# Kernel optimization log

Hardware: AMD Instinct MI355X
Metric: run time of the kernel (lower is better)

The kernel has to match this reference:

```python
import jax, jax.numpy as jnp
import numpy as np

N, E, G, B, L = 24576, 98304, 512, 512, 1000
F_IN, H1, C1, C2, HID = 5, 2, 64, 128, 256


def setup_inputs() -> dict:
    key = jax.random.key(0)
    ks = jax.random.split(key, 20)
    rn = lambda k, s: jax.random.normal(k, s, jnp.float32) * 0.1
    return {
        "x": jax.random.normal(ks[0], (N, F_IN), jnp.float32),
        "edge_index": jax.random.randint(ks[1], (2, E), 0, N),
        "batch": jnp.sort(jax.random.randint(ks[2], (N,), 0, G)),
        "protein_seq": jax.random.randint(ks[3], (B, L), 0, 22),
        "W1": rn(ks[4], (F_IN, H1 * C1)), "att_src1": rn(ks[5], (H1, C1)), "att_dst1": rn(ks[6], (H1, C1)), "b1": jnp.zeros((H1 * C1,), jnp.float32),
        "W2": rn(ks[7], (H1 * C1, C2)), "att_src2": rn(ks[8], (1, C2)), "att_dst2": rn(ks[9], (1, C2)), "b2": jnp.zeros((C2,), jnp.float32),
        "Wd": rn(ks[10], (C2, HID)), "bd": jnp.zeros((HID,), jnp.float32),
        "Pe": rn(ks[11], (22, 64)),
        "K1": rn(ks[12], (64, 64, 3)), "bk1": jnp.zeros((64,), jnp.float32),
        "K2": rn(ks[13], (128, 64, 5)), "bk2": jnp.zeros((128,), jnp.float32),
        "Wp": rn(ks[14], (128, HID)), "bp": jnp.zeros((HID,), jnp.float32),
        "Wf1": rn(ks[15], (2 * HID, 128)), "bf1": jnp.zeros((128,), jnp.float32),
        "Wf2": rn(ks[16], (128, 64)), "bf2": jnp.zeros((64,), jnp.float32),
        "Wo": rn(ks[17], (64, 1)), "bo": jnp.zeros((1,), jnp.float32),
    }


def _gat(x, edge_index, W, att_src, att_dst, b, heads, out_ch):
    """PyG GATConv: add self-loops, per-edge LeakyReLU(0.2) scores, segment softmax over dst."""
    n = x.shape[0]
    h = (x @ W).reshape(n, heads, out_ch)
    loop = jnp.arange(n)
    src = jnp.concatenate([edge_index[0], loop])
    dst = jnp.concatenate([edge_index[1], loop])
    a_s = jnp.sum(h * att_src[None], axis=-1)  # [n, H]
    a_d = jnp.sum(h * att_dst[None], axis=-1)
    e = jax.nn.leaky_relu(a_s[src] + a_d[dst], negative_slope=0.2)  # [E+n, H]
    m = jax.ops.segment_max(e, dst, num_segments=n)
    w = jnp.exp(e - m[dst])
    den = jax.ops.segment_sum(w, dst, num_segments=n)
    alpha = w / (den[dst] + 1e-16)
    out = jax.ops.segment_sum(h[src] * alpha[..., None], dst, num_segments=n)
    return out.reshape(n, heads * out_ch) + b


def _conv1d(x, k, pad):  # x: [B,C,L], k: [O,I,K]
    return jax.lax.conv_general_dilated(x, k, (1,), [(pad, pad)], dimension_numbers=("NCH", "OIH", "NCH"))


def reference(x, edge_index, batch, protein_seq, W1, att_src1, att_dst1, b1, W2, att_src2, att_dst2, b2, Wd, bd, Pe, K1, bk1, K2, bk2, Wp, bp, Wf1, bf1, Wf2, bf2, Wo, bo):
    # drug branch (GAT x2 + global mean pool)
    g = jax.nn.elu(_gat(x, edge_index, W1, att_src1, att_dst1, b1, H1, C1))
    g = jax.nn.elu(_gat(g, edge_index, W2, att_src2, att_dst2, b2, 1, C2))
    sums = jax.ops.segment_sum(g, batch, num_segments=G)
    cnt = jax.ops.segment_sum(jnp.ones((g.shape[0], 1), g.dtype), batch, num_segments=G)
    drug = jax.nn.relu(sums / jnp.maximum(cnt, 1.0) @ Wd + bd)
    # protein branch (embed -> conv1d x2 -> global max pool)
    pe = Pe[protein_seq].transpose(0, 2, 1)  # [B, 64, L]
    p = jax.nn.elu(_conv1d(pe, K1, 1) + bk1[None, :, None])
    p = jax.nn.elu(_conv1d(p, K2, 2) + bk2[None, :, None])
    prot = jax.nn.relu(jnp.max(p, axis=2) @ Wp + bp)
    # head
    h = jnp.concatenate([drug, prot], axis=1)
    h = jax.nn.relu(h @ Wf1 + bf1)
    h = jax.nn.relu(h @ Wf2 + bf2)
    return h @ Wo + bo
```

## Files before the change

### kernel.cpp

```cpp
#include <hip/hip_runtime.h>
#include <hip/hip_bf16.h>
#include <math.h>

#define NN 24576
#define NE 98304
#define ETOT (NE + NN)
#define NG 512
#define NB 512
#define LL 1000
#define TL 60
#define NTILE 17
#define PROT_BLKS (NB * NTILE)
#define CNT_BLKS (ETOT / 256)
#define AS1_BLKS (NN * 2 / 256)

typedef __attribute__((ext_vector_type(8))) short short8;
typedef __attribute__((ext_vector_type(4))) short short4v;
typedef __attribute__((ext_vector_type(4))) float f32x4;

__device__ inline short f2bf(float x) {
    union { __hip_bfloat16 b; short s; } u;
    u.b = __float2bfloat16(x);
    return u.s;
}

__device__ inline float bf2f(short s) {
    return __uint_as_float(((unsigned)(unsigned short)s) << 16);
}

__global__ void k_init_prep(int* deg, int* cursor, float* sums, float* cnt,
                            const float* K1, const float* K2, const float* W2, const float* Pe,
                            const float* W1, const float* as1c, const float* ad1c,
                            const float* as2c, const float* ad2c,
                            short* Bswz2, short* Bh2, short* Bl2, float* M1,
                            float* wvec) {
    int bid = blockIdx.x, t = threadIdx.x;
    if (bid < 256) {
        int i = bid * 256 + t;
        if (i < NN) { deg[i] = 0; cursor[i] = 0; }
        if (i < NG * 128) sums[i] = 0.f;
        if (i < NG) cnt[i] = 0.f;
        return;
    }
    int idx = (bid - 256) * 256 + t;
    if (idx < 20) {
        int q = idx % 10, hd = q / 5, f = q % 5;
        const float* av = (idx < 10) ? as1c : ad1c;
        float s = 0.f;
        for (int c = 0; c < 64; c++) s += W1[f * 128 + hd * 64 + c] * av[hd * 64 + c];
        wvec[idx < 10 ? q : 10 + q] = s;
    }
    if (idx >= 32 && idx < 288) {
        int q = idx - 32;
        int kk = q & 127;
        const float* av = (q < 128) ? as2c : ad2c;
        float s = 0.f;
        for (int n2 = 0; n2 < 128; n2++) s += W2[kk * 128 + n2] * av[n2];
        wvec[idx] = s;
    }
    if (idx < 22 * 3 * 64) {
        int tok = idx / 192, r2 = idx % 192;
        int k = r2 >> 6, oc = r2 & 63;
        float s = 0.f;
        for (int ic = 0; ic < 64; ic++) s += K1[oc * 192 + ic * 3 + k] * Pe[tok * 64 + ic];
        M1[idx] = s;
    }
    if (idx < 320 * 128) {
        int j = idx & 7, lane = (idx >> 3) & 63, rest = idx >> 9;
        int nt = rest & 7, kb = rest >> 3;
        int k = kb * 32 + ((lane >> 4) << 3) + j;
        int n = nt * 16 + (lane & 15);
        int kk = k / 64, i = k % 64;
        Bswz2[idx] = f2bf(K2[n * 320 + i * 5 + kk]);
    }
    if (idx < 128 * 128) {
        int j = idx & 7, lane = (idx >> 3) & 63, rest = idx >> 9;
        int nt = rest & 7, kb = rest >> 3;
        int k = kb * 32 + ((lane >> 4) << 3) + j;
        int n = nt * 16 + (lane & 15);
        float v = W2[k * 128 + n];
        short hh = f2bf(v);
        Bh2[idx] = hh;
        Bl2[idx] = f2bf(v - bf2f(hh));
    }
}

#define SSTR 72
__global__ __launch_bounds__(256, 6) void k_prot_cnt_as1(
    const int* seq, const float* M1, const float* bk1,
    const short* Bswz2, float* pmaxp,
    const int* ei, int* deg,
    const float* x, const float* wvec, float* rec) {
    int bid = blockIdx.x;
    int t = threadIdx.x;

    if (bid >= PROT_BLKS) {
        int rb = bid - PROT_BLKS;
        if (rb < CNT_BLKS) {
            int e = rb * 256 + t;
            int d = (e < NE) ? ei[NE + e] : e - NE;
            atomicAdd(&deg[d], 1);
        } else {
            int idx = (rb - CNT_BLKS) * 256 + t;
            int n = idx >> 1, hd = idx & 1;
            float xv[5];
            float s = 0.f, dv = 0.f;
#pragma unroll
            for (int f = 0; f < 5; f++) {
                xv[f] = x[n * 5 + f];
                s += xv[f] * wvec[hd * 5 + f];
                dv += xv[f] * wvec[10 + hd * 5 + f];
            }
            float* rr = &rec[n * 16];
            if (hd == 0) {
#pragma unroll
                for (int f = 0; f < 5; f++) rr[f] = xv[f];
                rr[5] = s; rr[7] = dv;
            } else {
                rr[6] = s; rr[8] = dv;
            }
        }
        return;
    }

    __shared__ __align__(16) short s1[68 * SSTR];

    int b = bid / NTILE;
    int tile = bid - b * NTILE;
    int t0 = tile * TL;

    if (t < 36) {
        *(short8*)&s1[64 * SSTR + t * 8] = (short8){0, 0, 0, 0, 0, 0, 0, 0};
    }

    {
        int q = t >> 2, c0 = (t & 3) << 4;
        int l = t0 - 2 + q;
        short tmp[16];
        if (l >= 0 && l < LL) {
            float v[16];
#pragma unroll
            for (int j = 0; j < 4; j++) {
                float4 bv = *(const float4*)&bk1[c0 + j * 4];
                v[j * 4 + 0] = bv.x; v[j * 4 + 1] = bv.y; v[j * 4 + 2] = bv.z; v[j * 4 + 3] = bv.w;
            }
#pragma unroll
            for (int k = 0; k < 3; k++) {
                int lp = l - 1 + k;
                if (lp >= 0 && lp < LL) {
                    int tok = seq[b * LL + lp];
                    const float4* mr = (const float4*)&M1[tok * 192 + k * 64 + c0];
#pragma unroll
                    for (int j = 0; j < 4; j++) {
                        float4 mv = mr[j];
                        v[j * 4 + 0] += mv.x; v[j * 4 + 1] += mv.y;
                        v[j * 4 + 2] += mv.z; v[j * 4 + 3] += mv.w;
                    }
                }
            }
#pragma unroll
            for (int j = 0; j < 16; j++) {
                float xv = v[j];
                xv = xv > 0.f ? xv : __expf(xv) - 1.f;
                tmp[j] = f2bf(xv);
            }
        } else {
#pragma unroll
            for (int j = 0; j < 16; j++) tmp[j] = 0;
        }
        *(short8*)&s1[q * SSTR + c0] = *(short8*)&tmp[0];
        *(short8*)&s1[q * SSTR + c0 + 8] = *(short8*)&tmp[8];
    }
    __syncthreads();

    int wv = t >> 6, lane = t & 63;
    int ln15 = lane & 15, quad = lane >> 4;

    f32x4 acc2[4][2];
#pragma unroll
    for (int mi = 0; mi < 4; mi++)
#pragma unroll
        for (int ni = 0; ni < 2; ni++) acc2[mi][ni] = (f32x4){0.f, 0.f, 0.f, 0.f};
#pragma unroll 2
    for (int kb = 0; kb < 10; kb++) {
        int koff = kb * 32 + quad * 8;
        int kk = koff >> 6, i0 = koff & 63;
        short8 a[4], bb[2];
#pragma unroll
        for (int mi = 0; mi < 4; mi++)
            a[mi] = *(const short8*)&s1[(mi * 16 + ln15 + kk) * SSTR + i0];
#pragma unroll
        for (int ni = 0; ni < 2; ni++)
            bb[ni] = *(const short8*)&Bswz2[((kb * 8 + wv * 2 + ni) * 64 + lane) * 8];
#pragma unroll
        for (int mi = 0; mi < 4; mi++)
#pragma unroll
            for (int ni = 0; ni < 2; ni++)
                acc2[mi][ni] = __builtin_amdgcn_mfma_f32_16x16x32_bf16(a[mi], bb[ni], acc2[mi][ni], 0, 0, 0);
    }

#pragma unroll
    for (int ni = 0; ni < 2; ni++) {
        int col = (wv * 2 + ni) * 16 + ln15;
        float mx = -1e30f;
#pragma unroll
        for (int mi = 0; mi < 4; mi++) {
#pragma unroll
            for (int r = 0; r < 4; r++) {
                int p = mi * 16 + quad * 4 + r;
                if (p < TL && t0 + p < LL) mx = fmaxf(mx, acc2[mi][ni][r]);
            }
        }
        mx = fmaxf(mx, __shfl_xor(mx, 16, 64));
        mx = fmaxf(mx, __shfl_xor(mx, 32, 64));
        if (quad == 0) pmaxp[(b * NTILE + tile) * 128 + col] = mx;
    }
}

__global__ void k_scan1(const int* deg, int* excl, int* part) {
    __shared__ int s[256];
    int b = blockIdx.x, t = threadIdx.x, i = b * 256 + t;
    int v = deg[i];
    s[t] = v;
    __syncthreads();
    for (int o = 1; o < 256; o <<= 1) {
        int x = (t >= o) ? s[t - o] : 0;
        __syncthreads();
        s[t] += x;
        __syncthreads();
    }
    excl[i] = s[t] - v;
    if (t == 255) part[b] = s[t];
}

__global__ void k_scan23(const int* excl, const int* part, int* rowptr) {
    __shared__ int sp[96];
    __shared__ int pref;
    int b = blockIdx.x, t = threadIdx.x;
    if (t < 96) sp[t] = part[t];
    __syncthreads();
    if (t == 0) {
        int run = 0;
        for (int i = 0; i < b; i++) run += sp[i];
        pref = run;
    }
    __syncthreads();
    int i = b * 256 + t;
    rowptr[i] = excl[i] + pref;
    if (i == 0) rowptr[NN] = ETOT;
}

__global__ void k_scatter(const int* ei, const int* rowptr, int* cursor, int* colidx) {
    int e = blockIdx.x * 256 + threadIdx.x;
    if (e >= ETOT) return;
    int s, d;
    if (e < NE) { s = ei[e]; d = ei[NE + e]; }
    else { s = d = e - NE; }
    int pos = atomicAdd(&cursor[d], 1);
    colidx[rowptr[d] + pos] = s;
}

__global__ void k_agg2x(const int* rowptr, const int* colidx, const float* rec,
                        const float* W1, const float* b1, const float* wvec,
                        unsigned int* g1b, float* as2, float* ad2) {
    __shared__ float sW[640];
    __shared__ float sb1[128];
    __shared__ float swa[256];
    int t = threadIdx.x;
    for (int i = t; i < 640; i += 256) sW[i] = W1[i];
    if (t < 128) { sb1[t] = b1[t]; swa[t] = wvec[32 + t]; swa[128 + t] = wvec[160 + t]; }
    __syncthreads();

    int d = blockIdx.x * 16 + (t >> 4);
    int g = t & 15;
    int hd = (g < 5) ? 0 : 1;
    int f = (g < 5) ? g : g - 5;
    float adv = rec[d * 16 + 7 + hd];
    int p0 = rowptr[d], p1 = rowptr[d + 1];
    float den = 0.f, acc = 0.f;
    if (g < 10) {
        for (int pc = p0; pc < p1; pc += 4) {
            int sarr[4]; float ev[4], xv[4];
#pragma unroll
            for (int i = 0; i < 4; i++) {
                int pp = pc + i;
                sarr[i] = colidx[pp < p1 ? pp : p1 - 1];
            }
#pragma unroll
            for (int i = 0; i < 4; i++) {
                ev[i] = rec[sarr[i] * 16 + 5 + hd];
                xv[i] = rec[sarr[i] * 16 + f];
            }
#pragma unroll
            for (int i = 0; i < 4; i++) {
                if (pc + i < p1) {
                    float e = ev[i] + adv;
                    e = e >= 0.f ? e : 0.2f * e;
                    float w = __expf(e);
                    den += w;
                    acc += w * xv[i];
                }
            }
        }
    }
    float xn = acc / (den + 1e-16f);
    int gb = (t & 63) & ~15;
    int hcol = g >> 3;
    float xs[5];
#pragma unroll
    for (int f2 = 0; f2 < 5; f2++)
        xs[f2] = __shfl(xn, gb + hcol * 5 + f2, 64);
    float ps = 0.f, pd = 0.f;
    float g1v[8];
#pragma unroll
    for (int k = 0; k < 8; k++) {
        int col = g * 8 + k;
        float v = sb1[col];
#pragma unroll
        for (int f2 = 0; f2 < 5; f2++) v += xs[f2] * sW[f2 * 128 + col];
        v = v > 0.f ? v : __expf(v) - 1.f;
        g1v[k] = v;
        ps += v * swa[col];
        pd += v * swa[128 + col];
    }
    uint4 pk;
    pk.x = ((unsigned)(unsigned short)f2bf(g1v[1]) << 16) | (unsigned)(unsigned short)f2bf(g1v[0]);
    pk.y = ((unsigned)(unsigned short)f2bf(g1v[3]) << 16) | (unsigned)(unsigned short)f2bf(g1v[2]);
    pk.z = ((unsigned)(unsigned short)f2bf(g1v[5]) << 16) | (unsigned)(unsigned short)f2bf(g1v[4]);
    pk.w = ((unsigned)(unsigned short)f2bf(g1v[7]) << 16) | (unsigned)(unsigned short)f2bf(g1v[6]);
    *(uint4*)&g1b[d * 64 + g * 4] = pk;
#pragma unroll
    for (int msk = 1; msk < 16; msk <<= 1) {
        ps += __shfl_xor(ps, msk, 64);
        pd += __shfl_xor(pd, msk, 64);
    }
    if (g == 0) { as2[d] = ps; ad2[d] = pd; }
}

__global__ void k_agg1y(const int* rowptr, const int* colidx, const unsigned int* hb,
                        const float* as_, const float* ad_, float* yacc) {
    int t = threadIdx.x;
    int d = blockIdx.x * 4 + (t >> 6);
    int c = t & 63;
    float adv = ad_[d];
    int p0 = rowptr[d], p1 = rowptr[d + 1];
    float den = 0.f, acc0 = 0.f, acc1 = 0.f;
    for (int pc = p0; pc < p1; pc += 4) {
        int sarr[4]; float ev[4]; unsigned int hv[4];
#pragma unroll
        for (int i = 0; i < 4; i++) {
            int pp = pc + i;
            sarr[i] = colidx[pp < p1 ? pp : p1 - 1];
        }
#pragma unroll
        for (int i = 0; i < 4; i++) {
            ev[i] = as_[sarr[i]];
            hv[i] = hb[sarr[i] * 64 + c];
        }
#pragma unroll
        for (int i = 0; i < 4; i++) {
            if (pc + i < p1) {
                float e = ev[i] + adv;
                e = e >= 0.f ? e : 0.2f * e;
                float w = __expf(e);
                den += w;
                acc0 += w * __uint_as_float(hv[i] << 16);
                acc1 += w * __uint_as_float(hv[i] & 0xFFFF0000u);
            }
        }
    }
    float inv = 1.f / (den + 1e-16f);
    ((float2*)yacc)[d * 64 + c] = (float2){acc0 * inv, acc1 * inv};
}

#define ASTR 136
__global__ __launch_bounds__(256, 2) void k_g2mm(
    const float* yacc, const short* Bh, const short* Bl, const float* b2, float* g2) {
    __shared__ __align__(16) short Ah[64 * ASTR];
    __shared__ __align__(16) short Al[64 * ASTR];
    int t = threadIdx.x;
    int m0 = blockIdx.x * 64;
    int wv = t >> 6, lane = t & 63;
    int ln15 = lane & 15, quad = lane >> 4;

    for (int i = t; i < 64 * 32; i += 256) {
        int row = i >> 5, c4 = (i & 31) * 4;
        float4 v = *(const float4*)&yacc[(m0 + row) * 128 + c4];
        short4v hi, lo;
        hi.x = f2bf(v.x); lo.x = f2bf(v.x - bf2f(hi.x));
        hi.y = f2bf(v.y); lo.y = f2bf(v.y - bf2f(hi.y));
        hi.z = f2bf(v.z); lo.z = f2bf(v.z - bf2f(hi.z));
        hi.w = f2bf(v.w); lo.w = f2bf(v.w - bf2f(hi.w));
        *(short4v*)&Ah[row * ASTR + c4] = hi;
        *(short4v*)&Al[row * ASTR + c4] = lo;
    }
    __syncthreads();

    f32x4 acc[8];
#pragma unroll
    for (int nt = 0; nt < 8; nt++) acc[nt] = (f32x4){0.f, 0.f, 0.f, 0.f};
    int arow = wv * 16 + ln15;
#pragma unroll
    for (int kb = 0; kb < 4; kb++) {
        int koff = kb * 32 + quad * 8;
        short8 a_hi = *(const short8*)&Ah[arow * ASTR + koff];
        short8 a_lo = *(const short8*)&Al[arow * ASTR + koff];
#pragma unroll
        for (int nt = 0; nt < 8; nt++) {
            short8 bh = *(const short8*)&Bh[((kb * 8 + nt) * 64 + lane) * 8];
            short8 bl = *(const short8*)&Bl[((kb * 8 + nt) * 64 + lane) * 8];
            acc[nt] = __builtin_amdgcn_mfma_f32_16x16x32_bf16(a_hi, bh, acc[nt], 0, 0, 0);
            acc[nt] = __builtin_amdgcn_mfma_f32_16x16x32_bf16(a_hi, bl, acc[nt], 0, 0, 0);
            acc[nt] = __builtin_amdgcn_mfma_f32_16x16x32_bf16(a_lo, bh, acc[nt], 0, 0, 0);
        }
    }
#pragma unroll
    for (int nt = 0; nt < 8; nt++) {
        int col = nt * 16 + ln15;
        float bias = b2[col];
#pragma unroll
        for (int r = 0; r < 4; r++) {
            float v = acc[nt][r] + bias;
            v = v > 0.f ? v : __expf(v) - 1.f;
            int n = m0 + wv * 16 + quad * 4 + r;
            g2[n * 128 + col] = v;
        }
    }
}

__global__ void k_pool(const float* g2, const int* batch, float* sums, float* cnt) {
    __shared__ int sb[96];
    int blk = blockIdx.x, j = threadIdx.x;
    int n0 = blk * 96;
    if (j < 96) sb[j] = batch[n0 + j];
    __syncthreads();
    float v[4];
#pragma unroll
    for (int i = 0; i < 4; i++) v[i] = g2[(n0 + i) * 128 + j];
    int cur = sb[0], runStart = 0;
    float acc = 0.f;
    for (int q0 = 0; q0 < 96; q0 += 4) {
        float nv[4] = {0.f, 0.f, 0.f, 0.f};
        if (q0 + 4 < 96) {
#pragma unroll
            for (int i = 0; i < 4; i++) nv[i] = g2[(n0 + q0 + 4 + i) * 128 + j];
        }
#pragma unroll
        for (int i = 0; i < 4; i++) {
            int q = q0 + i;
            int bb = sb[q];
            if (bb != cur) {
                atomicAdd(&sums[cur * 128 + j], acc);
                if (j == 0) atomicAdd(&cnt[cur], (float)(q - runStart));
                cur = bb; acc = 0.f; runStart = q;
            }
            acc += v[i];
        }
#pragma unroll
        for (int i = 0; i < 4; i++) v[i] = nv[i];
    }
    atomicAdd(&sums[cur * 128 + j], acc);
    if (j == 0) atomicAdd(&cnt[cur], (float)(96 - runStart));
}

__global__ __launch_bounds__(512) void k_tail(
    const float* pmaxp, const float* bk2, const float* Wp, const float* bp,
    const float* sums, const float* cnt, const float* Wd, const float* bd,
    const float* Wf1, const float* bf1, const float* Wf2, const float* bf2,
    const float* Wo, const float* bo, float* out) {
    __shared__ float spm[128];
    __shared__ float in2[512];
    __shared__ float part1[512];
    __shared__ float hh[128];
    __shared__ float part2[512];
    __shared__ float h2s[64];
    int g = blockIdx.x, t = threadIdx.x;

    if (t < 128) {
        float m = -1e30f;
#pragma unroll
        for (int tt = 0; tt < NTILE; tt++)
            m = fmaxf(m, pmaxp[(g * NTILE + tt) * 128 + t]);
        float v = m + bk2[t];
        spm[t] = v > 0.f ? v : __expf(v) - 1.f;
    }
    __syncthreads();

    if (t < 256) {
        float pacc = bp[t];
#pragma unroll 8
        for (int i = 0; i < 128; i++) pacc += spm[i] * Wp[i * 256 + t];
        in2[256 + t] = pacc > 0.f ? pacc : 0.f;
    } else {
        int o = t - 256;
        float c = cnt[g]; c = c < 1.f ? 1.f : c;
        float inv = 1.f / c;
        float dacc = bd[o];
#pragma unroll 8
        for (int i = 0; i < 128; i++) dacc += sums[g * 128 + i] * inv * Wd[i * 256 + o];
        in2[o] = dacc > 0.f ? dacc : 0.f;
    }
    __syncthreads();

    {
        int o = t >> 2, ks = t & 3;
        float p = 0.f;
        int c0 = ks * 128;
#pragma unroll 8
        for (int cc = c0; cc < c0 + 128; cc++) p += in2[cc] * Wf1[cc * 128 + o];
        part1[t] = p;
    }
    __syncthreads();
    if (t < 128) {
        float a = bf1[t] + part1[t * 4] + part1[t * 4 + 1] + part1[t * 4 + 2] + part1[t * 4 + 3];
        hh[t] = a > 0.f ? a : 0.f;
    }
    __syncthreads();

    {
        int o = t >> 3, ks = t & 7;
        float p = 0.f;
        int c0 = ks * 16;
#pragma unroll
        for (int cc = c0; cc < c0 + 16; cc++) p += hh[cc] * Wf2[cc * 64 + o];
        part2[t] = p;
    }
    __syncthreads();
    if (t < 64) {
        float a = bf2[t];
#pragma unroll
        for (int k = 0; k < 8; k++) a += part2[t * 8 + k];
        h2s[t] = a > 0.f ? a : 0.f;
    }
    __syncthreads();

    if (t < 64) {
        float p = h2s[t] * Wo[t];
#pragma unroll
        for (int off = 32; off > 0; off >>= 1) p += __shfl_down(p, off, 64);
        if (t == 0) out[g] = p + bo[0];
    }
}

extern "C" void kernel_launch(void* const* d_in, const int* in_sizes, int n_in,
                              void* d_out, int out_size, void* d_ws, size_t ws_size,
                              hipStream_t stream) {
    (void)in_sizes; (void)n_in; (void)out_size; (void)ws_size;
    const float* x   = (const float*)d_in[0];
    const int* ei    = (const int*)d_in[1];
    const int* batch = (const int*)d_in[2];
    const int* seq   = (const int*)d_in[3];
    const float* W1  = (const float*)d_in[4];
    const float* a_s1 = (const float*)d_in[5];
    const float* a_d1 = (const float*)d_in[6];
    const float* b1  = (const float*)d_in[7];
    const float* W2  = (const float*)d_in[8];
    const float* a_s2 = (const float*)d_in[9];
    const float* a_d2 = (const float*)d_in[10];
    const float* b2  = (const float*)d_in[11];
    const float* Wd  = (const float*)d_in[12];
    const float* bd  = (const float*)d_in[13];
    const float* Pe  = (const float*)d_in[14];
    const float* K1  = (const float*)d_in[15];
    const float* bk1 = (const float*)d_in[16];
    const float* K2  = (const float*)d_in[17];
    const float* bk2 = (const float*)d_in[18];
    const float* Wp  = (const float*)d_in[19];
    const float* bp  = (const float*)d_in[20];
    const float* Wf1 = (const float*)d_in[21];
    const float* bf1 = (const float*)d_in[22];
    const float* Wf2 = (const float*)d_in[23];
    const float* bf2 = (const float*)d_in[24];
    const float* Wo  = (const float*)d_in[25];
    const float* bo  = (const float*)d_in[26];
    float* out = (float*)d_out;

    float* w = (float*)d_ws;
    float* g1bf = w; w += NN * 64;
    float* yacc = w; w += NN * 128;
    float* g2   = w; w += NN * 128;
    float* as2  = w; w += NN;
    float* ad2  = w; w += NN;
    float* sums = w; w += NG * 128;
    float* cnt  = w; w += NG;
    float* pmaxp = w; w += NB * NTILE * 128;
    float* rec  = w; w += NN * 16;
    float* wvec = w; w += 512;
    short* Bswz2 = (short*)w; w += 320 * 128 / 2;
    short* Bh2  = (short*)w; w += 128 * 128 / 2;
    short* Bl2  = (short*)w; w += 128 * 128 / 2;
    float* M1   = w; w += 22 * 3 * 64;
    int* deg    = (int*)w; w += NN;
    int* cursor = (int*)w; w += NN;
    int* excl   = (int*)w; w += NN;
    int* part   = (int*)w; w += 128;
    int* rowptr = (int*)w; w += NN + 8;
    int* colidx = (int*)w; w += ETOT;

    unsigned int* g1b = (unsigned int*)g1bf;

    hipLaunchKernelGGL(k_init_prep, dim3(256 + 160), dim3(256), 0, stream,
                       deg, cursor, sums, cnt,
                       K1, K2, W2, Pe, W1, a_s1, a_d1, a_s2, a_d2,
                       Bswz2, Bh2, Bl2, M1, wvec);

    hipLaunchKernelGGL(k_prot_cnt_as1, dim3(PROT_BLKS + CNT_BLKS + AS1_BLKS), dim3(256), 0, stream,
                       seq, M1, bk1, Bswz2, pmaxp,
                       ei, deg, x, wvec, rec);

    hipLaunchKernelGGL(k_scan1, dim3(NN / 256), dim3(256), 0, stream, deg, excl, part);
    hipLaunchKernelGGL(k_scan23, dim3(NN / 256), dim3(256), 0, stream, excl, part, rowptr);
    hipLaunchKernelGGL(k_scatter, dim3(ETOT / 256), dim3(256), 0, stream, ei, rowptr, cursor, colidx);

    hipLaunchKernelGGL(k_agg2x, dim3(NN / 16), dim3(256), 0, stream,
                       rowptr, colidx, rec, W1, b1, wvec, g1b, as2, ad2);

    hipLaunchKernelGGL(k_agg1y, dim3(NN / 4), dim3(256), 0, stream,
                       rowptr, colidx, g1b, as2, ad2, yacc);

    hipLaunchKernelGGL(k_g2mm, dim3(NN / 64), dim3(256), 0, stream,
                       yacc, Bh2, Bl2, b2, g2);

    hipLaunchKernelGGL(k_pool, dim3(NN / 96), dim3(128), 0, stream, g2, batch, sums, cnt);

    hipLaunchKernelGGL(k_tail, dim3(NG), dim3(512), 0, stream,
                       pmaxp, bk2, Wp, bp, sums, cnt, Wd, bd, Wf1, bf1, Wf2, bf2, Wo, bo, out);
}
```

Baseline: 271.4 us.

## Process two protein conv tiles per block to reuse B fragments

Each protein-conv block now handles two adjacent 60-position tiles instead of one. Both tiles go into a doubled shared buffer, and each loaded K2 weight fragment feeds twice as many MFMAs. This halves the protein block count and the global weight loads per output, but raises register pressure (the accumulators double), so the occupancy hint drops from 6 to 4. With 17 tiles per sequence, the last pair has one empty tile that still does its compute.

```diff
diff --git a/kernel.cpp b/kernel.cpp
--- a/kernel.cpp
+++ b/kernel.cpp
@@ -10,7 +10,8 @@
 #define LL 1000
 #define TL 60
 #define NTILE 17
-#define PROT_BLKS (NB * NTILE)
+#define PPAIR 9
+#define PROT_BLKS (NB * PPAIR)
 #define CNT_BLKS (ETOT / 256)
 #define AS1_BLKS (NN * 2 / 256)
 
@@ -86,7 +87,7 @@
 }
 
 #define SSTR 72
-__global__ __launch_bounds__(256, 6) void k_prot_cnt_as1(
+__global__ __launch_bounds__(256, 4) void k_prot_cnt_as1(
     const int* seq, const float* M1, const float* bk1,
     const short* Bswz2, float* pmaxp,
     const int* ei, int* deg,
@@ -123,21 +124,27 @@
         return;
     }
 
-    __shared__ __align__(16) short s1[68 * SSTR];
-
-    int b = bid / NTILE;
-    int tile = bid - b * NTILE;
-    int t0 = tile * TL;
-
-    if (t < 36) {
-        *(short8*)&s1[64 * SSTR + t * 8] = (short8){0, 0, 0, 0, 0, 0, 0, 0};
-    }
-
-    {
-        int q = t >> 2, c0 = (t & 3) << 4;
-        int l = t0 - 2 + q;
+    __shared__ __align__(16) short s1[2 * 68 * SSTR];
+
+    int b = bid / PPAIR;
+    int u = bid - b * PPAIR;
+    int tile0 = u * 2;
+
+    for (int i = t; i < 2 * 4 * SSTR; i += 256) {
+        int zr = i / SSTR, zc = i - zr * SSTR;
+        int row = (zr >> 2) * 68 + 64 + (zr & 3);
+        s1[row * SSTR + zc] = 0;
+    }
+
+#pragma unroll
+    for (int uu = 0; uu < 2; uu++) {
+        int un = t + uu * 256;
+        int row = un >> 2, c0 = (un & 3) << 4;
+        int tt = row >> 6, q = row & 63;
+        int tile = tile0 + tt;
+        int l = tile * TL - 2 + q;
         short tmp[16];
-        if (l >= 0 && l < LL) {
+        if (tile < NTILE && l >= 0 && l < LL) {
             float v[16];
 #pragma unroll
             for (int j = 0; j < 4; j++) {
@@ -168,52 +175,58 @@
 #pragma unroll
             for (int j = 0; j < 16; j++) tmp[j] = 0;
         }
-        *(short8*)&s1[q * SSTR + c0] = *(short8*)&tmp[0];
-        *(short8*)&s1[q * SSTR + c0 + 8] = *(short8*)&tmp[8];
+        *(short8*)&s1[(tt * 68 + q) * SSTR + c0] = *(short8*)&tmp[0];
+        *(short8*)&s1[(tt * 68 + q) * SSTR + c0 + 8] = *(short8*)&tmp[8];
     }
     __syncthreads();
 
     int wv = t >> 6, lane = t & 63;
     int ln15 = lane & 15, quad = lane >> 4;
 
-    f32x4 acc2[4][2];
-#pragma unroll
-    for (int mi = 0; mi < 4; mi++)
+    f32x4 acc2[8][2];
+#pragma unroll
+    for (int mi = 0; mi < 8; mi++)
 #pragma unroll
         for (int ni = 0; ni < 2; ni++) acc2[mi][ni] = (f32x4){0.f, 0.f, 0.f, 0.f};
 #pragma unroll 2
     for (int kb = 0; kb < 10; kb++) {
         int koff = kb * 32 + quad * 8;
         int kk = koff >> 6, i0 = koff & 63;
-        short8 a[4], bb[2];
-#pragma unroll
-        for (int mi = 0; mi < 4; mi++)
-            a[mi] = *(const short8*)&s1[(mi * 16 + ln15 + kk) * SSTR + i0];
+        short8 bb[2];
 #pragma unroll
         for (int ni = 0; ni < 2; ni++)
             bb[ni] = *(const short8*)&Bswz2[((kb * 8 + wv * 2 + ni) * 64 + lane) * 8];
 #pragma unroll
-        for (int mi = 0; mi < 4; mi++)
-#pragma unroll
-            for (int ni = 0; ni < 2; ni++)
-                acc2[mi][ni] = __builtin_amdgcn_mfma_f32_16x16x32_bf16(a[mi], bb[ni], acc2[mi][ni], 0, 0, 0);
+        for (int mi = 0; mi < 8; mi++) {
+            int row = (mi >> 2) * 68 + (mi & 3) * 16 + ln15 + kk;
+            short8 a = *(const short8*)&s1[row * SSTR + i0];
+            acc2[mi][0] = __builtin_amdgcn_mfma_f32_16x16x32_bf16(a, bb[0], acc2[mi][0], 0, 0, 0);
+            acc2[mi][1] = __builtin_amdgcn_mfma_f32_16x16x32_bf16(a, bb[1], acc2[mi][1], 0, 0, 0);
+        }
     }
 
 #pragma unroll
     for (int ni = 0; ni < 2; ni++) {
         int col = (wv * 2 + ni) * 16 + ln15;
-        float mx = -1e30f;
-#pragma unroll
-        for (int mi = 0; mi < 4; mi++) {
-#pragma unroll
-            for (int r = 0; r < 4; r++) {
-                int p = mi * 16 + quad * 4 + r;
-                if (p < TL && t0 + p < LL) mx = fmaxf(mx, acc2[mi][ni][r]);
-            }
-        }
-        mx = fmaxf(mx, __shfl_xor(mx, 16, 64));
-        mx = fmaxf(mx, __shfl_xor(mx, 32, 64));
-        if (quad == 0) pmaxp[(b * NTILE + tile) * 128 + col] = mx;
+#pragma unroll
+        for (int tt = 0; tt < 2; tt++) {
+            int tile = tile0 + tt;
+            int t0 = tile * TL;
+            float mx = -1e30f;
+#pragma unroll
+            for (int mj = 0; mj < 4; mj++) {
+                int mi = tt * 4 + mj;
+#pragma unroll
+                for (int r = 0; r < 4; r++) {
+                    int p = mj * 16 + quad * 4 + r;
+                    if (p < TL && t0 + p < LL) mx = fmaxf(mx, acc2[mi][ni][r]);
+                }
+            }
+            mx = fmaxf(mx, __shfl_xor(mx, 16, 64));
+            mx = fmaxf(mx, __shfl_xor(mx, 32, 64));
+            if (quad == 0 && tile < NTILE)
+                pmaxp[(b * NTILE + tile) * 128 + col] = mx;
+        }
     }
 }
 
```

Measured after the change: 276.0 us. About the same (+1.7%).

## Fuse mean-pool into GAT2 matmul epilogue and fold conv1 bias into table

Applied to the files above, without the earlier changes.

Drops the separate pooling kernel and the g2 intermediate buffer. The k_g2mm epilogue now accumulates per-graph partial sums in registers and sends them to the pooled sums with atomics. Node counts per graph move into the as1 branch as atomics, and bk1 is folded into the precomputed M1 table. The block order in the fused prot kernel puts the cheap count and as1 blocks first, and the conv2 k-loop is fully unrolled. This trades a full N×128 write and re-read plus one launch for many more atomicAdds, one per 4-row run per column per wave.

```diff
diff --git a/kernel.cpp b/kernel.cpp
--- a/kernel.cpp
+++ b/kernel.cpp
@@ -31,7 +31,7 @@
 __global__ void k_init_prep(int* deg, int* cursor, float* sums, float* cnt,
                             const float* K1, const float* K2, const float* W2, const float* Pe,
                             const float* W1, const float* as1c, const float* ad1c,
-                            const float* as2c, const float* ad2c,
+                            const float* as2c, const float* ad2c, const float* bk1,
                             short* Bswz2, short* Bh2, short* Bl2, float* M1,
                             float* wvec) {
     int bid = blockIdx.x, t = threadIdx.x;
@@ -61,7 +61,7 @@
     if (idx < 22 * 3 * 64) {
         int tok = idx / 192, r2 = idx % 192;
         int k = r2 >> 6, oc = r2 & 63;
-        float s = 0.f;
+        float s = (k == 1) ? bk1[oc] : 0.f;
         for (int ic = 0; ic < 64; ic++) s += K1[oc * 192 + ic * 3 + k] * Pe[tok * 64 + ic];
         M1[idx] = s;
     }
@@ -87,46 +87,47 @@
 
 #define SSTR 72
 __global__ __launch_bounds__(256, 6) void k_prot_cnt_as1(
-    const int* seq, const float* M1, const float* bk1,
+    const int* seq, const float* M1,
     const short* Bswz2, float* pmaxp,
-    const int* ei, int* deg,
+    const int* ei, int* deg, const int* batch, float* cnt,
     const float* x, const float* wvec, float* rec) {
     int bid = blockIdx.x;
     int t = threadIdx.x;
 
-    if (bid >= PROT_BLKS) {
-        int rb = bid - PROT_BLKS;
-        if (rb < CNT_BLKS) {
-            int e = rb * 256 + t;
-            int d = (e < NE) ? ei[NE + e] : e - NE;
-            atomicAdd(&deg[d], 1);
+    if (bid < CNT_BLKS) {
+        int e = bid * 256 + t;
+        int d = (e < NE) ? ei[NE + e] : e - NE;
+        atomicAdd(&deg[d], 1);
+        return;
+    }
+    if (bid < CNT_BLKS + AS1_BLKS) {
+        int idx = (bid - CNT_BLKS) * 256 + t;
+        int n = idx >> 1, hd = idx & 1;
+        float xv[5];
+        float s = 0.f, dv = 0.f;
+#pragma unroll
+        for (int f = 0; f < 5; f++) {
+            xv[f] = x[n * 5 + f];
+            s += xv[f] * wvec[hd * 5 + f];
+            dv += xv[f] * wvec[10 + hd * 5 + f];
+        }
+        float* rr = &rec[n * 16];
+        if (hd == 0) {
+#pragma unroll
+            for (int f = 0; f < 5; f++) rr[f] = xv[f];
+            rr[5] = s; rr[7] = dv;
+            atomicAdd(&cnt[batch[n]], 1.f);
         } else {
-            int idx = (rb - CNT_BLKS) * 256 + t;
-            int n = idx >> 1, hd = idx & 1;
-            float xv[5];
-            float s = 0.f, dv = 0.f;
-#pragma unroll
-            for (int f = 0; f < 5; f++) {
-                xv[f] = x[n * 5 + f];
-                s += xv[f] * wvec[hd * 5 + f];
-                dv += xv[f] * wvec[10 + hd * 5 + f];
-            }
-            float* rr = &rec[n * 16];
-            if (hd == 0) {
-#pragma unroll
-                for (int f = 0; f < 5; f++) rr[f] = xv[f];
-                rr[5] = s; rr[7] = dv;
-            } else {
-                rr[6] = s; rr[8] = dv;
-            }
+            rr[6] = s; rr[8] = dv;
         }
         return;
     }
 
     __shared__ __align__(16) short s1[68 * SSTR];
 
-    int b = bid / NTILE;
-    int tile = bid - b * NTILE;
+    int pb = bid - (CNT_BLKS + AS1_BLKS);
+    int b = pb / NTILE;
+    int tile = pb - b * NTILE;
     int t0 = tile * TL;
 
     if (t < 36) {
@@ -140,10 +141,7 @@
         if (l >= 0 && l < LL) {
             float v[16];
 #pragma unroll
-            for (int j = 0; j < 4; j++) {
-                float4 bv = *(const float4*)&bk1[c0 + j * 4];
-                v[j * 4 + 0] = bv.x; v[j * 4 + 1] = bv.y; v[j * 4 + 2] = bv.z; v[j * 4 + 3] = bv.w;
-            }
+            for (int j = 0; j < 16; j++) v[j] = 0.f;
 #pragma unroll
             for (int k = 0; k < 3; k++) {
                 int lp = l - 1 + k;
@@ -181,7 +179,7 @@
     for (int mi = 0; mi < 4; mi++)
 #pragma unroll
         for (int ni = 0; ni < 2; ni++) acc2[mi][ni] = (f32x4){0.f, 0.f, 0.f, 0.f};
-#pragma unroll 2
+#pragma unroll
     for (int kb = 0; kb < 10; kb++) {
         int koff = kb * 32 + quad * 8;
         int kk = koff >> 6, i0 = koff & 63;
@@ -375,14 +373,17 @@
 
 #define ASTR 136
 __global__ __launch_bounds__(256, 2) void k_g2mm(
-    const float* yacc, const short* Bh, const short* Bl, const float* b2, float* g2) {
+    const float* yacc, const short* Bh, const short* Bl, const float* b2,
+    const int* batch, float* sums) {
     __shared__ __align__(16) short Ah[64 * ASTR];
     __shared__ __align__(16) short Al[64 * ASTR];
+    __shared__ int sb[64];
     int t = threadIdx.x;
     int m0 = blockIdx.x * 64;
     int wv = t >> 6, lane = t & 63;
     int ln15 = lane & 15, quad = lane >> 4;
 
+    if (t < 64) sb[t] = batch[m0 + t];
     for (int i = t; i < 64 * 32; i += 256) {
         int row = i >> 5, c4 = (i & 31) * 4;
         float4 v = *(const float4*)&yacc[(m0 + row) * 128 + c4];
@@ -414,53 +415,26 @@
             acc[nt] = __builtin_amdgcn_mfma_f32_16x16x32_bf16(a_lo, bh, acc[nt], 0, 0, 0);
         }
     }
+    int rbase = wv * 16 + quad * 4;
 #pragma unroll
     for (int nt = 0; nt < 8; nt++) {
         int col = nt * 16 + ln15;
         float bias = b2[col];
+        float run = 0.f;
+        int cg = sb[rbase];
 #pragma unroll
         for (int r = 0; r < 4; r++) {
             float v = acc[nt][r] + bias;
             v = v > 0.f ? v : __expf(v) - 1.f;
-            int n = m0 + wv * 16 + quad * 4 + r;
-            g2[n * 128 + col] = v;
-        }
-    }
-}
-
-__global__ void k_pool(const float* g2, const int* batch, float* sums, float* cnt) {
-    __shared__ int sb[96];
-    int blk = blockIdx.x, j = threadIdx.x;
-    int n0 = blk * 96;
-    if (j < 96) sb[j] = batch[n0 + j];
-    __syncthreads();
-    float v[4];
-#pragma unroll
-    for (int i = 0; i < 4; i++) v[i] = g2[(n0 + i) * 128 + j];
-    int cur = sb[0], runStart = 0;
-    float acc = 0.f;
-    for (int q0 = 0; q0 < 96; q0 += 4) {
-        float nv[4] = {0.f, 0.f, 0.f, 0.f};
-        if (q0 + 4 < 96) {
-#pragma unroll
-            for (int i = 0; i < 4; i++) nv[i] = g2[(n0 + q0 + 4 + i) * 128 + j];
-        }
-#pragma unroll
-        for (int i = 0; i < 4; i++) {
-            int q = q0 + i;
-            int bb = sb[q];
-            if (bb != cur) {
-                atomicAdd(&sums[cur * 128 + j], acc);
-                if (j == 0) atomicAdd(&cnt[cur], (float)(q - runStart));
-                cur = bb; acc = 0.f; runStart = q;
-            }
-            acc += v[i];
-        }
-#pragma unroll
-        for (int i = 0; i < 4; i++) v[i] = nv[i];
-    }
-    atomicAdd(&sums[cur * 128 + j], acc);
-    if (j == 0) atomicAdd(&cnt[cur], (float)(96 - runStart));
+            int g = sb[rbase + r];
+            if (g != cg) {
+                atomicAdd(&sums[cg * 128 + col], run);
+                run = 0.f; cg = g;
+            }
+            run += v;
+        }
+        atomicAdd(&sums[cg * 128 + col], run);
+    }
 }
 
 __global__ __launch_bounds__(512) void k_tail(
@@ -578,7 +552,6 @@
     float* w = (float*)d_ws;
     float* g1bf = w; w += NN * 64;
     float* yacc = w; w += NN * 128;
-    float* g2   = w; w += NN * 128;
     float* as2  = w; w += NN;
     float* ad2  = w; w += NN;
     float* sums = w; w += NG * 128;
@@ -601,12 +574,12 @@
 
     hipLaunchKernelGGL(k_init_prep, dim3(256 + 160), dim3(256), 0, stream,
                        deg, cursor, sums, cnt,
-                       K1, K2, W2, Pe, W1, a_s1, a_d1, a_s2, a_d2,
+                       K1, K2, W2, Pe, W1, a_s1, a_d1, a_s2, a_d2, bk1,
                        Bswz2, Bh2, Bl2, M1, wvec);
 
-    hipLaunchKernelGGL(k_prot_cnt_as1, dim3(PROT_BLKS + CNT_BLKS + AS1_BLKS), dim3(256), 0, stream,
-                       seq, M1, bk1, Bswz2, pmaxp,
-                       ei, deg, x, wvec, rec);
+    hipLaunchKernelGGL(k_prot_cnt_as1, dim3(CNT_BLKS + AS1_BLKS + PROT_BLKS), dim3(256), 0, stream,
+                       seq, M1, Bswz2, pmaxp,
+                       ei, deg, batch, cnt, x, wvec, rec);
 
     hipLaunchKernelGGL(k_scan1, dim3(NN / 256), dim3(256), 0, stream, deg, excl, part);
     hipLaunchKernelGGL(k_scan23, dim3(NN / 256), dim3(256), 0, stream, excl, part, rowptr);
@@ -619,9 +592,7 @@
                        rowptr, colidx, g1b, as2, ad2, yacc);
 
     hipLaunchKernelGGL(k_g2mm, dim3(NN / 64), dim3(256), 0, stream,
-                       yacc, Bh2, Bl2, b2, g2);
-
-    hipLaunchKernelGGL(k_pool, dim3(NN / 96), dim3(128), 0, stream, g2, batch, sums, cnt);
+                       yacc, Bh2, Bl2, b2, batch, sums);
 
     hipLaunchKernelGGL(k_tail, dim3(NG), dim3(512), 0, stream,
                        pmaxp, bk2, Wp, bp, sums, cnt, Wd, bd, Wf1, bf1, Wf2, bf2, Wo, bo, out);
```

New measurement: 282.6 us. +4.1%, slower.
